# Performance work log

Hardware: AMD Instinct MI355X
Metric: run time of the kernel (lower is better)

Reference implementation:

```python
import jax, jax.numpy as jnp
import numpy as np

B, T, C = 8, 1024, 576
NH, NKV = 9, 3          # query heads, kv heads
HD = C // NH            # 64 head dim
KVC = C // NKV          # 192 kv proj width
N_REP = NH // NKV       # 3


def setup_inputs() -> dict:
    key = jax.random.key(0)
    ks = jax.random.split(key, 9)
    s = 0.02
    return {
        "x": jax.random.normal(ks[0], (B, T, C), jnp.float32),
        "Wq": jax.random.normal(ks[1], (C, C), jnp.float32) * s,
        "bq": jax.random.normal(ks[2], (C,), jnp.float32) * s,
        "Wk": jax.random.normal(ks[3], (C, KVC), jnp.float32) * s,
        "bk": jax.random.normal(ks[4], (KVC,), jnp.float32) * s,
        "Wv": jax.random.normal(ks[5], (C, KVC), jnp.float32) * s,
        "bv": jax.random.normal(ks[6], (KVC,), jnp.float32) * s,
        "Wo": jax.random.normal(ks[7], (C, C), jnp.float32) * s,
        "bo": jax.random.normal(ks[8], (C,), jnp.float32) * s,
    }


def reference(x, Wq, bq, Wk, bk, Wv, bv, Wo, bo):
    Bx, Tx, Cx = x.shape
    q = x @ Wq + bq                                # [B,T,C]
    k = x @ Wk + bk                                # [B,T,KVC]
    v = x @ Wv + bv
    # split heads: q -> [B,NH,T,HD]; k,v -> [B,NKV,T,HD]
    q = q.reshape(Bx, Tx, NH, HD).transpose(0, 2, 1, 3)
    k = k.reshape(Bx, Tx, NKV, HD).transpose(0, 2, 1, 3)
    v = v.reshape(Bx, Tx, NKV, HD).transpose(0, 2, 1, 3)
    # repeat_kv: [B,NKV,T,HD] -> [B,NKV*N_REP,T,HD]
    k = jnp.repeat(k, N_REP, axis=1)
    v = jnp.repeat(v, N_REP, axis=1)
    att = jnp.einsum("bhqd,bhkd->bhqk", q, k) * (1.0 / np.sqrt(HD))
    mask = jnp.tril(jnp.ones((Tx, Tx), bool))
    att = jnp.where(mask, att, -jnp.inf)
    att = jax.nn.softmax(att, axis=-1)
    y = jnp.einsum("bhqk,bhkd->bhqd", att, v)      # [B,NH,T,HD]
    y = y.transpose(0, 2, 1, 3).reshape(Bx, Tx, Cx)
    return y @ Wo + bo
```

## Files before the change

### kernel.cpp

```cpp
#include <hip/hip_runtime.h>
#include <hip/hip_bf16.h>
#include <math.h>

#define B_    8
#define T_    1024
#define C_    576
#define NH_   9
#define NKV_  3
#define HD_   64
#define KVC_  192
#define NREP_ 3
#define NQKV_ 960
#define NTK_  9

typedef __attribute__((ext_vector_type(8))) short bf16x8;
typedef __attribute__((ext_vector_type(4))) float f32x4;
typedef __attribute__((ext_vector_type(4))) int i32x4;

#define MFMA_16x16x32(a, b, c) __builtin_amdgcn_mfma_f32_16x16x32_bf16((a), (b), (c), 0, 0, 0)

__device__ __forceinline__ ushort f2bf(float f) {
  __hip_bfloat16 h = __float2bfloat16(f);
  return *reinterpret_cast<const ushort*>(&h);
}

__device__ __forceinline__ float fexp2(float x) { return __builtin_amdgcn_exp2f(x); }

__device__ __forceinline__ int swz(int row, int col) {
  int byte = (row << 7) + (col << 1);
  return (byte ^ ((row & 7) << 4)) >> 1;
}

__device__ __forceinline__ void gload16(const ushort* g, ushort* l) {
  __builtin_amdgcn_global_load_lds(
      (const __attribute__((address_space(1))) unsigned int*)g,
      (__attribute__((address_space(3))) unsigned int*)l, 16, 0, 0);
}

__device__ __forceinline__ i32x4 packrow(const float* src) {
  const float4 a = *reinterpret_cast<const float4*>(src);
  const float4 b = *reinterpret_cast<const float4*>(src + 4);
  union { ushort u[8]; i32x4 v; } t;
  t.u[0] = f2bf(a.x); t.u[1] = f2bf(a.y); t.u[2] = f2bf(a.z); t.u[3] = f2bf(a.w);
  t.u[4] = f2bf(b.x); t.u[5] = f2bf(b.y); t.u[6] = f2bf(b.z); t.u[7] = f2bf(b.w);
  return t.v;
}

__global__ __launch_bounds__(256) void convert_x_kernel(
    const float* __restrict__ x, ushort* __restrict__ xbt) {
  const int tm = blockIdx.x, tk = blockIdx.y;
  ushort* dst = xbt + ((size_t)tm * NTK_ + tk) * 8192;
  #pragma unroll
  for (int i = 0; i < 4; i++) {
    const int c = threadIdx.x + i * 256;
    const int row = c >> 3, colb = (c & 7) * 8;
    *reinterpret_cast<i32x4*>(&dst[swz(row, colb)]) =
        packrow(x + (size_t)(tm * 128 + row) * C_ + tk * 64 + colb);
  }
}

__global__ __launch_bounds__(256) void convert_w_kernel(
    const float* __restrict__ Wq, const float* __restrict__ Wk,
    const float* __restrict__ Wv, const float* __restrict__ Wo,
    const float* __restrict__ bq, const float* __restrict__ bk,
    const float* __restrict__ bv, const float* __restrict__ bo,
    ushort* __restrict__ wqkvT, ushort* __restrict__ woT, float* __restrict__ bcat) {
  const int tnc = blockIdx.x, tk = blockIdx.y;
  #pragma unroll
  for (int i = 0; i < 2; i++) {
    const int c = threadIdx.x + i * 256;
    const int row = c >> 3, colb = (c & 7) * 8;
    const float* src; int ld; ushort* dst; int ncol;
    if (tnc < 15) {
      const int n = tnc * 64 + row;
      if (n < 576)      { src = Wq; ld = C_;  ncol = n; }
      else if (n < 768) { src = Wk; ld = KVC_; ncol = n - 576; }
      else              { src = Wv; ld = KVC_; ncol = n - 768; }
      dst = wqkvT + ((size_t)tnc * NTK_ + tk) * 4096;
    } else {
      src = Wo; ld = C_; ncol = (tnc - 15) * 64 + row;
      dst = woT + ((size_t)(tnc - 15) * NTK_ + tk) * 4096;
    }
    union { ushort u[8]; i32x4 v; } t;
    #pragma unroll
    for (int e = 0; e < 8; e++)
      t.u[e] = f2bf(src[(size_t)(tk * 64 + colb + e) * ld + ncol]);
    *reinterpret_cast<i32x4*>(&dst[swz(row, colb)]) = t.v;
    if (tk == 0 && (c & 7) == 0) {
      const int n = tnc * 64 + row;
      float bv_;
      if (n < 576)       bv_ = bq[n];
      else if (n < 768)  bv_ = bk[n - 576];
      else if (n < 960)  bv_ = bv[n - 768];
      else               bv_ = bo[n - 960];
      bcat[n] = bv_;
    }
  }
}

template<int MODE>
__global__ __launch_bounds__(256) void gemm_lds_kernel(
    const ushort* __restrict__ At, const ushort* __restrict__ Bt,
    const float* __restrict__ bias, void* __restrict__ Cp,
    ushort* __restrict__ ktv, ushort* __restrict__ vtv, int N) {
  const int nwg = gridDim.x * gridDim.y;
  const int flat = blockIdx.y * gridDim.x + blockIdx.x;
  const int wg = (flat & 7) * (nwg >> 3) + (flat >> 3);
  const int bxs = wg % gridDim.x, bys = wg / gridDim.x;

  __shared__ ushort As[128 * 64];
  __shared__ ushort Bs[64 * 64];
  const int bm = bys * 128, bn = bxs * 64;
  const int tid = threadIdx.x;
  const int wave = tid >> 6, lane = tid & 63;
  const int lg = lane >> 4, ll = lane & 15;
  const int wm = (wave >> 1) * 64, wn = (wave & 1) * 32;
  f32x4 acc[4][2] = {};

  const ushort* abase = At + (size_t)bys * NTK_ * 8192;
  const ushort* bbase = Bt + (size_t)bxs * NTK_ * 4096;

  for (int kt = 0; kt < NTK_; kt++) {
    const ushort* ak = abase + (size_t)kt * 8192;
    const ushort* bk = bbase + (size_t)kt * 4096;
    #pragma unroll
    for (int i = 0; i < 4; i++) {
      const int c0 = (wave << 6) + (i << 8);
      gload16(ak + (size_t)(c0 + lane) * 8, &As[c0 * 8]);
    }
    #pragma unroll
    for (int i = 0; i < 2; i++) {
      const int c0 = (wave << 6) + (i << 8);
      gload16(bk + (size_t)(c0 + lane) * 8, &Bs[c0 * 8]);
    }
    __syncthreads();

    bf16x8 af[4][2], bfr[2][2];
    #pragma unroll
    for (int mt = 0; mt < 4; mt++) {
      af[mt][0] = *reinterpret_cast<const bf16x8*>(&As[swz(wm + mt * 16 + ll, lg * 8)]);
      af[mt][1] = *reinterpret_cast<const bf16x8*>(&As[swz(wm + mt * 16 + ll, 32 + lg * 8)]);
    }
    #pragma unroll
    for (int nt = 0; nt < 2; nt++) {
      bfr[nt][0] = *reinterpret_cast<const bf16x8*>(&Bs[swz(wn + nt * 16 + ll, lg * 8)]);
      bfr[nt][1] = *reinterpret_cast<const bf16x8*>(&Bs[swz(wn + nt * 16 + ll, 32 + lg * 8)]);
    }
    #pragma unroll
    for (int mt = 0; mt < 4; mt++) {
      #pragma unroll
      for (int nt = 0; nt < 2; nt++) {
        acc[mt][nt] = MFMA_16x16x32(af[mt][0], bfr[nt][0], acc[mt][nt]);
        acc[mt][nt] = MFMA_16x16x32(af[mt][1], bfr[nt][1], acc[mt][nt]);
      }
    }
    __syncthreads();
  }

  #pragma unroll
  for (int mt = 0; mt < 4; mt++) {
    #pragma unroll
    for (int nt = 0; nt < 2; nt++) {
      const int col = bn + wn + nt * 16 + ll;
      #pragma unroll
      for (int r = 0; r < 4; r++) {
        const int row = bm + wm + mt * 16 + lg * 4 + r;
        const float val = acc[mt][nt][r] + bias[col];
        if (MODE == 0) {
          ((float*)Cp)[(size_t)row * N + col] = val;
        } else {
          if (col < 576) {
            ((ushort*)Cp)[(size_t)row * C_ + col] = f2bf(val * 0.18033688011112042f);
          } else if (col < 768) {
            const int kvh = (col - 576) >> 6, d = (col - 576) & 63;
            ushort* t = ktv + (((size_t)(row >> 10) * 3 + kvh) * 16 + ((row >> 6) & 15)) * 4096;
            t[swz(row & 63, d)] = f2bf(val);
          } else {
            const int kvh = (col - 768) >> 6, d = (col - 768) & 63;
            ushort* t = vtv + (((size_t)(row >> 10) * 3 + kvh) * 16 + ((row >> 6) & 15)) * 4096;
            t[swz(d, row & 63)] = f2bf(val);
          }
        }
      }
    }
  }
}

__global__ __launch_bounds__(256) void attn_mfma_kernel(
    const ushort* __restrict__ qb, const ushort* __restrict__ ktv,
    const ushort* __restrict__ vtv, ushort* __restrict__ yt) {
  const int qt = 15 - blockIdx.z, h = blockIdx.x, b = blockIdx.y;
  const int kvh = h / NREP_;
  const int tid = threadIdx.x;
  const int wave = tid >> 6, lane = tid & 63;
  const int lg = lane >> 4, ll = lane & 15;
  const int w16 = wave << 4;
  const int qrow0 = qt << 6;
  const int ntile = qt + 1;

  __shared__ ushort Ks[2][4096];
  __shared__ ushort Vts[2][4096];
  __shared__ ushort Ps[4][1024];

  const ushort* ktb = ktv + ((size_t)b * 3 + kvh) * 16 * 4096;
  const ushort* vtb = vtv + ((size_t)b * 3 + kvh) * 16 * 4096;

  const ushort* qrow = qb + (size_t)(b * T_ + qrow0 + w16 + ll) * C_ + h * HD_;
  const bf16x8 qa0 = *reinterpret_cast<const bf16x8*>(qrow + lg * 8);
  const bf16x8 qa1 = *reinterpret_cast<const bf16x8*>(qrow + 32 + lg * 8);

  f32x4 o[4] = {};
  float m_i = -INFINITY, l_i = 0.f;

  {
    const ushort* ks = ktb;
    const ushort* vs = vtb;
    #pragma unroll
    for (int i = 0; i < 2; i++) {
      const int c0 = (wave << 6) + (i << 8);
      gload16(ks + (size_t)(c0 + lane) * 8, &Ks[0][c0 * 8]);
      gload16(vs + (size_t)(c0 + lane) * 8, &Vts[0][c0 * 8]);
    }
  }

  #pragma unroll 1
  for (int t = 0; t < ntile; t++) {
    const int cur = t & 1;
    if (t + 1 < ntile) {
      const ushort* ks = ktb + (size_t)(t + 1) * 4096;
      const ushort* vs = vtb + (size_t)(t + 1) * 4096;
      #pragma unroll
      for (int i = 0; i < 2; i++) {
        const int c0 = (wave << 6) + (i << 8);
        gload16(ks + (size_t)(c0 + lane) * 8, &Ks[cur ^ 1][c0 * 8]);
        gload16(vs + (size_t)(c0 + lane) * 8, &Vts[cur ^ 1][c0 * 8]);
      }
      asm volatile("s_waitcnt vmcnt(4)" ::: "memory");
    } else {
      asm volatile("s_waitcnt vmcnt(0)" ::: "memory");
    }
    __builtin_amdgcn_s_barrier();

    f32x4 s[4];
    #pragma unroll
    for (int kcl = 0; kcl < 4; kcl++) {
      const bf16x8 kb0 = *reinterpret_cast<const bf16x8*>(&Ks[cur][swz(kcl * 16 + ll, lg * 8)]);
      const bf16x8 kb1 = *reinterpret_cast<const bf16x8*>(&Ks[cur][swz(kcl * 16 + ll, 32 + lg * 8)]);
      f32x4 z = {};
      z = MFMA_16x16x32(kb0, qa0, z);
      s[kcl] = MFMA_16x16x32(kb1, qa1, z);
    }

    if (t == ntile - 1) {
      const int qg = qrow0 + w16 + ll - (t << 6);
      #pragma unroll
      for (int kcl = 0; kcl < 4; kcl++)
        #pragma unroll
        for (int r = 0; r < 4; r++)
          if (kcl * 16 + lg * 4 + r > qg) s[kcl][r] = -INFINITY;
    }

    float mA[4];
    #pragma unroll
    for (int kcl = 0; kcl < 4; kcl++)
      mA[kcl] = fmaxf(fmaxf(s[kcl][0], s[kcl][1]), fmaxf(s[kcl][2], s[kcl][3]));
    float t0 = fmaxf(fmaxf(mA[0], mA[1]), fmaxf(mA[2], mA[3]));
    t0 = fmaxf(t0, __shfl_xor(t0, 16));
    t0 = fmaxf(t0, __shfl_xor(t0, 32));
    if (!__all(t0 <= m_i + 11.5415603f)) {
      const float mn = fmaxf(m_i, t0);
      const float al = fexp2(m_i - mn);
      m_i = mn;
      l_i *= al;
      #pragma unroll
      for (int r = 0; r < 4; r++) {
        const float ar = __shfl(al, lg * 4 + r);
        o[0][r] *= ar; o[1][r] *= ar; o[2][r] *= ar; o[3][r] *= ar;
      }
    }

    float rk[4];
    ushort* Pw = Ps[wave];
    #pragma unroll
    for (int kcl = 0; kcl < 4; kcl++) {
      float p0 = fexp2(s[kcl][0] - m_i);
      float p1 = fexp2(s[kcl][1] - m_i);
      float p2 = fexp2(s[kcl][2] - m_i);
      float p3 = fexp2(s[kcl][3] - m_i);
      rk[kcl] = (p0 + p1) + (p2 + p3);
      uint w01 = (uint)f2bf(p0) | ((uint)f2bf(p1) << 16);
      uint w23 = (uint)f2bf(p2) | ((uint)f2bf(p3) << 16);
      *reinterpret_cast<uint*>(&Pw[swz(ll, kcl * 16 + lg * 4)])     = w01;
      *reinterpret_cast<uint*>(&Pw[swz(ll, kcl * 16 + lg * 4 + 2)]) = w23;
    }
    #pragma unroll
    for (int khl = 0; khl < 2; khl++) {
      const bf16x8 pa = *reinterpret_cast<const bf16x8*>(&Pw[swz(ll, khl * 32 + lg * 8)]);
      #pragma unroll
      for (int d0 = 0; d0 < 4; d0++) {
        const bf16x8 vbr = *reinterpret_cast<const bf16x8*>(&Vts[cur][swz(d0 * 16 + ll, khl * 32 + lg * 8)]);
        o[d0] = MFMA_16x16x32(pa, vbr, o[d0]);
      }
    }
    float rs = (rk[0] + rk[1]) + (rk[2] + rk[3]);
    rs += __shfl_xor(rs, 16);
    rs += __shfl_xor(rs, 32);
    l_i += rs;

    __builtin_amdgcn_s_barrier();
  }

  #pragma unroll
  for (int r = 0; r < 4; r++) {
    const float lr = __shfl(l_i, lg * 4 + r);
    const float inv = 1.f / lr;
    const int rowg = b * T_ + qrow0 + w16 + lg * 4 + r;
    ushort* ybase = yt + ((size_t)(rowg >> 7) * NTK_ + h) * 8192;
    const int lrow = rowg & 127;
    #pragma unroll
    for (int d0 = 0; d0 < 4; d0++) {
      ybase[swz(lrow, d0 * 16 + ll)] = f2bf(o[d0][r] * inv);
    }
  }
}

extern "C" void kernel_launch(void* const* d_in, const int* in_sizes, int n_in,
                              void* d_out, int out_size, void* d_ws, size_t ws_size,
                              hipStream_t stream) {
  const float* x  = (const float*)d_in[0];
  const float* Wq = (const float*)d_in[1];
  const float* bq = (const float*)d_in[2];
  const float* Wk = (const float*)d_in[3];
  const float* bk = (const float*)d_in[4];
  const float* Wv = (const float*)d_in[5];
  const float* bv = (const float*)d_in[6];
  const float* Wo = (const float*)d_in[7];
  const float* bo = (const float*)d_in[8];
  float* out = (float*)d_out;

  const int M = B_ * T_;
  ushort* wqkvT = (ushort*)d_ws;
  ushort* woT   = wqkvT + (size_t)15 * NTK_ * 4096;
  float*  bcat  = (float*)(woT + (size_t)9 * NTK_ * 4096);
  ushort* qb    = (ushort*)(bcat + 1536);
  ushort* ktv   = qb + (size_t)M * C_;
  ushort* vtv   = ktv + (size_t)B_ * NKV_ * 16 * 4096;
  ushort* yt    = vtv + (size_t)B_ * NKV_ * 16 * 4096;
  ushort* xbt   = yt + (size_t)M * C_;

  convert_w_kernel<<<dim3(24, NTK_), 256, 0, stream>>>(Wq, Wk, Wv, Wo, bq, bk, bv, bo,
                                                       wqkvT, woT, bcat);
  convert_x_kernel<<<dim3(M / 128, NTK_), 256, 0, stream>>>(x, xbt);
  gemm_lds_kernel<1><<<dim3(NQKV_ / 64, M / 128), 256, 0, stream>>>(
      xbt, wqkvT, bcat, qb, ktv, vtv, NQKV_);
  attn_mfma_kernel<<<dim3(NH_, B_, 16), 256, 0, stream>>>(qb, ktv, vtv, yt);
  gemm_lds_kernel<0><<<dim3(C_ / 64, M / 128), 256, 0, stream>>>(
      yt, woT, bcat + NQKV_, out, nullptr, nullptr, C_);
}
```

Before: 70.65 us.

## Double-buffer LDS tiles in projection GEMM to overlap loads with MFMA

```diff
diff --git a/kernel.cpp b/kernel.cpp
--- a/kernel.cpp
+++ b/kernel.cpp
@@ -108,8 +108,8 @@
   const int wg = (flat & 7) * (nwg >> 3) + (flat >> 3);
   const int bxs = wg % gridDim.x, bys = wg / gridDim.x;
 
-  __shared__ ushort As[128 * 64];
-  __shared__ ushort Bs[64 * 64];
+  __shared__ ushort As[2][128 * 64];
+  __shared__ ushort Bs[2][64 * 64];
   const int bm = bys * 128, bn = bxs * 64;
   const int tid = threadIdx.x;
   const int wave = tid >> 6, lane = tid & 63;
@@ -120,31 +120,50 @@
   const ushort* abase = At + (size_t)bys * NTK_ * 8192;
   const ushort* bbase = Bt + (size_t)bxs * NTK_ * 4096;
 
-  for (int kt = 0; kt < NTK_; kt++) {
-    const ushort* ak = abase + (size_t)kt * 8192;
-    const ushort* bk = bbase + (size_t)kt * 4096;
+  {
     #pragma unroll
     for (int i = 0; i < 4; i++) {
       const int c0 = (wave << 6) + (i << 8);
-      gload16(ak + (size_t)(c0 + lane) * 8, &As[c0 * 8]);
+      gload16(abase + (size_t)(c0 + lane) * 8, &As[0][c0 * 8]);
     }
     #pragma unroll
     for (int i = 0; i < 2; i++) {
       const int c0 = (wave << 6) + (i << 8);
-      gload16(bk + (size_t)(c0 + lane) * 8, &Bs[c0 * 8]);
-    }
-    __syncthreads();
+      gload16(bbase + (size_t)(c0 + lane) * 8, &Bs[0][c0 * 8]);
+    }
+  }
+
+  for (int kt = 0; kt < NTK_; kt++) {
+    const int cur = kt & 1;
+    if (kt + 1 < NTK_) {
+      const ushort* ak = abase + (size_t)(kt + 1) * 8192;
+      const ushort* bk = bbase + (size_t)(kt + 1) * 4096;
+      #pragma unroll
+      for (int i = 0; i < 4; i++) {
+        const int c0 = (wave << 6) + (i << 8);
+        gload16(ak + (size_t)(c0 + lane) * 8, &As[cur ^ 1][c0 * 8]);
+      }
+      #pragma unroll
+      for (int i = 0; i < 2; i++) {
+        const int c0 = (wave << 6) + (i << 8);
+        gload16(bk + (size_t)(c0 + lane) * 8, &Bs[cur ^ 1][c0 * 8]);
+      }
+      asm volatile("s_waitcnt vmcnt(6)" ::: "memory");
+    } else {
+      asm volatile("s_waitcnt vmcnt(0)" ::: "memory");
+    }
+    __builtin_amdgcn_s_barrier();
 
     bf16x8 af[4][2], bfr[2][2];
     #pragma unroll
     for (int mt = 0; mt < 4; mt++) {
-      af[mt][0] = *reinterpret_cast<const bf16x8*>(&As[swz(wm + mt * 16 + ll, lg * 8)]);
-      af[mt][1] = *reinterpret_cast<const bf16x8*>(&As[swz(wm + mt * 16 + ll, 32 + lg * 8)]);
+      af[mt][0] = *reinterpret_cast<const bf16x8*>(&As[cur][swz(wm + mt * 16 + ll, lg * 8)]);
+      af[mt][1] = *reinterpret_cast<const bf16x8*>(&As[cur][swz(wm + mt * 16 + ll, 32 + lg * 8)]);
     }
     #pragma unroll
     for (int nt = 0; nt < 2; nt++) {
-      bfr[nt][0] = *reinterpret_cast<const bf16x8*>(&Bs[swz(wn + nt * 16 + ll, lg * 8)]);
-      bfr[nt][1] = *reinterpret_cast<const bf16x8*>(&Bs[swz(wn + nt * 16 + ll, 32 + lg * 8)]);
+      bfr[nt][0] = *reinterpret_cast<const bf16x8*>(&Bs[cur][swz(wn + nt * 16 + ll, lg * 8)]);
+      bfr[nt][1] = *reinterpret_cast<const bf16x8*>(&Bs[cur][swz(wn + nt * 16 + ll, 32 + lg * 8)]);
     }
     #pragma unroll
     for (int mt = 0; mt < 4; mt++) {
@@ -154,7 +173,7 @@
         acc[mt][nt] = MFMA_16x16x32(af[mt][1], bfr[nt][1], acc[mt][nt]);
       }
     }
-    __syncthreads();
+    __builtin_amdgcn_s_barrier();
   }
 
   #pragma unroll
```

Result: no change. 71.13 us (+0.7%).

## Fuse conversion kernels and remap attention blocks for per-XCD KV locality

Applied to the files above, without the earlier changes.

```diff
diff --git a/kernel.cpp b/kernel.cpp
--- a/kernel.cpp
+++ b/kernel.cpp
@@ -46,54 +46,57 @@
   return t.v;
 }
 
-__global__ __launch_bounds__(256) void convert_x_kernel(
-    const float* __restrict__ x, ushort* __restrict__ xbt) {
-  const int tm = blockIdx.x, tk = blockIdx.y;
-  ushort* dst = xbt + ((size_t)tm * NTK_ + tk) * 8192;
-  #pragma unroll
-  for (int i = 0; i < 4; i++) {
-    const int c = threadIdx.x + i * 256;
-    const int row = c >> 3, colb = (c & 7) * 8;
-    *reinterpret_cast<i32x4*>(&dst[swz(row, colb)]) =
-        packrow(x + (size_t)(tm * 128 + row) * C_ + tk * 64 + colb);
-  }
-}
-
-__global__ __launch_bounds__(256) void convert_w_kernel(
+__global__ __launch_bounds__(256) void convert_all_kernel(
+    const float* __restrict__ x,
     const float* __restrict__ Wq, const float* __restrict__ Wk,
     const float* __restrict__ Wv, const float* __restrict__ Wo,
     const float* __restrict__ bq, const float* __restrict__ bk,
     const float* __restrict__ bv, const float* __restrict__ bo,
-    ushort* __restrict__ wqkvT, ushort* __restrict__ woT, float* __restrict__ bcat) {
-  const int tnc = blockIdx.x, tk = blockIdx.y;
-  #pragma unroll
-  for (int i = 0; i < 2; i++) {
-    const int c = threadIdx.x + i * 256;
-    const int row = c >> 3, colb = (c & 7) * 8;
-    const float* src; int ld; ushort* dst; int ncol;
-    if (tnc < 15) {
-      const int n = tnc * 64 + row;
-      if (n < 576)      { src = Wq; ld = C_;  ncol = n; }
-      else if (n < 768) { src = Wk; ld = KVC_; ncol = n - 576; }
-      else              { src = Wv; ld = KVC_; ncol = n - 768; }
-      dst = wqkvT + ((size_t)tnc * NTK_ + tk) * 4096;
-    } else {
-      src = Wo; ld = C_; ncol = (tnc - 15) * 64 + row;
-      dst = woT + ((size_t)(tnc - 15) * NTK_ + tk) * 4096;
-    }
-    union { ushort u[8]; i32x4 v; } t;
-    #pragma unroll
-    for (int e = 0; e < 8; e++)
-      t.u[e] = f2bf(src[(size_t)(tk * 64 + colb + e) * ld + ncol]);
-    *reinterpret_cast<i32x4*>(&dst[swz(row, colb)]) = t.v;
-    if (tk == 0 && (c & 7) == 0) {
-      const int n = tnc * 64 + row;
-      float bv_;
-      if (n < 576)       bv_ = bq[n];
-      else if (n < 768)  bv_ = bk[n - 576];
-      else if (n < 960)  bv_ = bv[n - 768];
-      else               bv_ = bo[n - 960];
-      bcat[n] = bv_;
+    ushort* __restrict__ wqkvT, ushort* __restrict__ woT, float* __restrict__ bcat,
+    ushort* __restrict__ xbt) {
+  const int bid = blockIdx.x;
+  if (bid < 216) {
+    const int tnc = bid / 9, tk = bid % 9;
+    #pragma unroll
+    for (int i = 0; i < 2; i++) {
+      const int c = threadIdx.x + i * 256;
+      const int row = c >> 3, colb = (c & 7) * 8;
+      const float* src; int ld; ushort* dst; int ncol;
+      if (tnc < 15) {
+        const int n = tnc * 64 + row;
+        if (n < 576)      { src = Wq; ld = C_;  ncol = n; }
+        else if (n < 768) { src = Wk; ld = KVC_; ncol = n - 576; }
+        else              { src = Wv; ld = KVC_; ncol = n - 768; }
+        dst = wqkvT + ((size_t)tnc * NTK_ + tk) * 4096;
+      } else {
+        src = Wo; ld = C_; ncol = (tnc - 15) * 64 + row;
+        dst = woT + ((size_t)(tnc - 15) * NTK_ + tk) * 4096;
+      }
+      union { ushort u[8]; i32x4 v; } t;
+      #pragma unroll
+      for (int e = 0; e < 8; e++)
+        t.u[e] = f2bf(src[(size_t)(tk * 64 + colb + e) * ld + ncol]);
+      *reinterpret_cast<i32x4*>(&dst[swz(row, colb)]) = t.v;
+      if (tk == 0 && (c & 7) == 0) {
+        const int n = tnc * 64 + row;
+        float bv_;
+        if (n < 576)       bv_ = bq[n];
+        else if (n < 768)  bv_ = bk[n - 576];
+        else if (n < 960)  bv_ = bv[n - 768];
+        else               bv_ = bo[n - 960];
+        bcat[n] = bv_;
+      }
+    }
+  } else {
+    const int r = bid - 216;
+    const int tm = r / 9, tk = r % 9;
+    ushort* dst = xbt + ((size_t)tm * NTK_ + tk) * 8192;
+    #pragma unroll
+    for (int i = 0; i < 4; i++) {
+      const int c = threadIdx.x + i * 256;
+      const int row = c >> 3, colb = (c & 7) * 8;
+      *reinterpret_cast<i32x4*>(&dst[swz(row, colb)]) =
+          packrow(x + (size_t)(tm * 128 + row) * C_ + tk * 64 + colb);
     }
   }
 }
@@ -189,8 +192,14 @@
 __global__ __launch_bounds__(256) void attn_mfma_kernel(
     const ushort* __restrict__ qb, const ushort* __restrict__ ktv,
     const ushort* __restrict__ vtv, ushort* __restrict__ yt) {
-  const int qt = 15 - blockIdx.z, h = blockIdx.x, b = blockIdx.y;
-  const int kvh = h / NREP_;
+  const int f = blockIdx.x + NH_ * (blockIdx.y + B_ * blockIdx.z);
+  const int xcd = f & 7, chunk = f >> 3;
+  const int g = xcd * 3 + chunk / 48;
+  const int within = chunk % 48;
+  const int b = g & 7, kvh = g >> 3;
+  const int h = kvh * 3 + within % 3;
+  const int qt = 15 - within / 3;
+
   const int tid = threadIdx.x;
   const int wave = tid >> 6, lane = tid & 63;
   const int lg = lane >> 4, ll = lane & 15;
@@ -213,13 +222,11 @@
   float m_i = -INFINITY, l_i = 0.f;
 
   {
-    const ushort* ks = ktb;
-    const ushort* vs = vtb;
     #pragma unroll
     for (int i = 0; i < 2; i++) {
       const int c0 = (wave << 6) + (i << 8);
-      gload16(ks + (size_t)(c0 + lane) * 8, &Ks[0][c0 * 8]);
-      gload16(vs + (size_t)(c0 + lane) * 8, &Vts[0][c0 * 8]);
+      gload16(ktb + (size_t)(c0 + lane) * 8, &Ks[0][c0 * 8]);
+      gload16(vtb + (size_t)(c0 + lane) * 8, &Vts[0][c0 * 8]);
     }
   }
 
@@ -348,9 +355,8 @@
   ushort* yt    = vtv + (size_t)B_ * NKV_ * 16 * 4096;
   ushort* xbt   = yt + (size_t)M * C_;
 
-  convert_w_kernel<<<dim3(24, NTK_), 256, 0, stream>>>(Wq, Wk, Wv, Wo, bq, bk, bv, bo,
-                                                       wqkvT, woT, bcat);
-  convert_x_kernel<<<dim3(M / 128, NTK_), 256, 0, stream>>>(x, xbt);
+  convert_all_kernel<<<dim3(216 + 576), 256, 0, stream>>>(
+      x, Wq, Wk, Wv, Wo, bq, bk, bv, bo, wqkvT, woT, bcat, xbt);
   gemm_lds_kernel<1><<<dim3(NQKV_ / 64, M / 128), 256, 0, stream>>>(
       xbt, wqkvT, bcat, qb, ktv, vtv, NQKV_);
   attn_mfma_kernel<<<dim3(NH_, B_, 16), 256, 0, stream>>>(qb, ktv, vtv, yt);
```

Measured after the change: 73.86 us. 1.05x slower.

## Make attention kernel persistent with an atomic work queue, heaviest tiles first

Applied to the files above, without the earlier changes.

```diff
diff --git a/kernel.cpp b/kernel.cpp
--- a/kernel.cpp
+++ b/kernel.cpp
@@ -12,6 +12,7 @@
 #define NREP_ 3
 #define NQKV_ 960
 #define NTK_  9
+#define NITEM_ 1152
 
 typedef __attribute__((ext_vector_type(8))) short bf16x8;
 typedef __attribute__((ext_vector_type(4))) float f32x4;
@@ -64,8 +65,10 @@
     const float* __restrict__ Wv, const float* __restrict__ Wo,
     const float* __restrict__ bq, const float* __restrict__ bk,
     const float* __restrict__ bv, const float* __restrict__ bo,
-    ushort* __restrict__ wqkvT, ushort* __restrict__ woT, float* __restrict__ bcat) {
+    ushort* __restrict__ wqkvT, ushort* __restrict__ woT, float* __restrict__ bcat,
+    uint* __restrict__ qcount) {
   const int tnc = blockIdx.x, tk = blockIdx.y;
+  if (tnc == 0 && tk == 0 && threadIdx.x == 0) *qcount = 0u;
   #pragma unroll
   for (int i = 0; i < 2; i++) {
     const int c = threadIdx.x + i * 256;
@@ -188,138 +191,145 @@
 
 __global__ __launch_bounds__(256) void attn_mfma_kernel(
     const ushort* __restrict__ qb, const ushort* __restrict__ ktv,
-    const ushort* __restrict__ vtv, ushort* __restrict__ yt) {
-  const int qt = 15 - blockIdx.z, h = blockIdx.x, b = blockIdx.y;
-  const int kvh = h / NREP_;
+    const ushort* __restrict__ vtv, ushort* __restrict__ yt,
+    uint* __restrict__ qcount) {
   const int tid = threadIdx.x;
   const int wave = tid >> 6, lane = tid & 63;
   const int lg = lane >> 4, ll = lane & 15;
   const int w16 = wave << 4;
-  const int qrow0 = qt << 6;
-  const int ntile = qt + 1;
 
   __shared__ ushort Ks[2][4096];
   __shared__ ushort Vts[2][4096];
   __shared__ ushort Ps[4][1024];
-
-  const ushort* ktb = ktv + ((size_t)b * 3 + kvh) * 16 * 4096;
-  const ushort* vtb = vtv + ((size_t)b * 3 + kvh) * 16 * 4096;
-
-  const ushort* qrow = qb + (size_t)(b * T_ + qrow0 + w16 + ll) * C_ + h * HD_;
-  const bf16x8 qa0 = *reinterpret_cast<const bf16x8*>(qrow + lg * 8);
-  const bf16x8 qa1 = *reinterpret_cast<const bf16x8*>(qrow + 32 + lg * 8);
-
-  f32x4 o[4] = {};
-  float m_i = -INFINITY, l_i = 0.f;
-
-  {
-    const ushort* ks = ktb;
-    const ushort* vs = vtb;
+  __shared__ uint witem;
+
+  while (true) {
+    if (tid == 0) witem = atomicAdd(qcount, 1u);
+    __syncthreads();
+    const uint w = witem;
+    if (w >= NITEM_) break;
+    const int qt = 15 - (int)(w / 72);
+    const int rem = (int)(w % 72);
+    const int h = rem % 9, b = rem / 9;
+    const int kvh = h / NREP_;
+    const int qrow0 = qt << 6;
+    const int ntile = qt + 1;
+
+    const ushort* ktb = ktv + ((size_t)b * 3 + kvh) * 16 * 4096;
+    const ushort* vtb = vtv + ((size_t)b * 3 + kvh) * 16 * 4096;
+
+    const ushort* qrow = qb + (size_t)(b * T_ + qrow0 + w16 + ll) * C_ + h * HD_;
+    const bf16x8 qa0 = *reinterpret_cast<const bf16x8*>(qrow + lg * 8);
+    const bf16x8 qa1 = *reinterpret_cast<const bf16x8*>(qrow + 32 + lg * 8);
+
+    f32x4 o[4] = {};
+    float m_i = -INFINITY, l_i = 0.f;
+
     #pragma unroll
     for (int i = 0; i < 2; i++) {
       const int c0 = (wave << 6) + (i << 8);
-      gload16(ks + (size_t)(c0 + lane) * 8, &Ks[0][c0 * 8]);
-      gload16(vs + (size_t)(c0 + lane) * 8, &Vts[0][c0 * 8]);
-    }
-  }
-
-  #pragma unroll 1
-  for (int t = 0; t < ntile; t++) {
-    const int cur = t & 1;
-    if (t + 1 < ntile) {
-      const ushort* ks = ktb + (size_t)(t + 1) * 4096;
-      const ushort* vs = vtb + (size_t)(t + 1) * 4096;
-      #pragma unroll
-      for (int i = 0; i < 2; i++) {
-        const int c0 = (wave << 6) + (i << 8);
-        gload16(ks + (size_t)(c0 + lane) * 8, &Ks[cur ^ 1][c0 * 8]);
-        gload16(vs + (size_t)(c0 + lane) * 8, &Vts[cur ^ 1][c0 * 8]);
-      }
-      asm volatile("s_waitcnt vmcnt(4)" ::: "memory");
-    } else {
-      asm volatile("s_waitcnt vmcnt(0)" ::: "memory");
-    }
-    __builtin_amdgcn_s_barrier();
-
-    f32x4 s[4];
-    #pragma unroll
-    for (int kcl = 0; kcl < 4; kcl++) {
-      const bf16x8 kb0 = *reinterpret_cast<const bf16x8*>(&Ks[cur][swz(kcl * 16 + ll, lg * 8)]);
-      const bf16x8 kb1 = *reinterpret_cast<const bf16x8*>(&Ks[cur][swz(kcl * 16 + ll, 32 + lg * 8)]);
-      f32x4 z = {};
-      z = MFMA_16x16x32(kb0, qa0, z);
-      s[kcl] = MFMA_16x16x32(kb1, qa1, z);
-    }
-
-    if (t == ntile - 1) {
-      const int qg = qrow0 + w16 + ll - (t << 6);
+      gload16(ktb + (size_t)(c0 + lane) * 8, &Ks[0][c0 * 8]);
+      gload16(vtb + (size_t)(c0 + lane) * 8, &Vts[0][c0 * 8]);
+    }
+
+    #pragma unroll 1
+    for (int t = 0; t < ntile; t++) {
+      const int cur = t & 1;
+      if (t + 1 < ntile) {
+        const ushort* ks = ktb + (size_t)(t + 1) * 4096;
+        const ushort* vs = vtb + (size_t)(t + 1) * 4096;
+        #pragma unroll
+        for (int i = 0; i < 2; i++) {
+          const int c0 = (wave << 6) + (i << 8);
+          gload16(ks + (size_t)(c0 + lane) * 8, &Ks[cur ^ 1][c0 * 8]);
+          gload16(vs + (size_t)(c0 + lane) * 8, &Vts[cur ^ 1][c0 * 8]);
+        }
+        asm volatile("s_waitcnt vmcnt(4)" ::: "memory");
+      } else {
+        asm volatile("s_waitcnt vmcnt(0)" ::: "memory");
+      }
+      __builtin_amdgcn_s_barrier();
+
+      f32x4 s[4];
+      #pragma unroll
+      for (int kcl = 0; kcl < 4; kcl++) {
+        const bf16x8 kb0 = *reinterpret_cast<const bf16x8*>(&Ks[cur][swz(kcl * 16 + ll, lg * 8)]);
+        const bf16x8 kb1 = *reinterpret_cast<const bf16x8*>(&Ks[cur][swz(kcl * 16 + ll, 32 + lg * 8)]);
+        f32x4 z = {};
+        z = MFMA_16x16x32(kb0, qa0, z);
+        s[kcl] = MFMA_16x16x32(kb1, qa1, z);
+      }
+
+      if (t == ntile - 1) {
+        const int qg = qrow0 + w16 + ll - (t << 6);
+        #pragma unroll
+        for (int kcl = 0; kcl < 4; kcl++)
+          #pragma unroll
+          for (int r = 0; r < 4; r++)
+            if (kcl * 16 + lg * 4 + r > qg) s[kcl][r] = -INFINITY;
+      }
+
+      float mA[4];
       #pragma unroll
       for (int kcl = 0; kcl < 4; kcl++)
+        mA[kcl] = fmaxf(fmaxf(s[kcl][0], s[kcl][1]), fmaxf(s[kcl][2], s[kcl][3]));
+      float t0 = fmaxf(fmaxf(mA[0], mA[1]), fmaxf(mA[2], mA[3]));
+      t0 = fmaxf(t0, __shfl_xor(t0, 16));
+      t0 = fmaxf(t0, __shfl_xor(t0, 32));
+      if (!__all(t0 <= m_i + 11.5415603f)) {
+        const float mn = fmaxf(m_i, t0);
+        const float al = fexp2(m_i - mn);
+        m_i = mn;
+        l_i *= al;
         #pragma unroll
-        for (int r = 0; r < 4; r++)
-          if (kcl * 16 + lg * 4 + r > qg) s[kcl][r] = -INFINITY;
-    }
-
-    float mA[4];
-    #pragma unroll
-    for (int kcl = 0; kcl < 4; kcl++)
-      mA[kcl] = fmaxf(fmaxf(s[kcl][0], s[kcl][1]), fmaxf(s[kcl][2], s[kcl][3]));
-    float t0 = fmaxf(fmaxf(mA[0], mA[1]), fmaxf(mA[2], mA[3]));
-    t0 = fmaxf(t0, __shfl_xor(t0, 16));
-    t0 = fmaxf(t0, __shfl_xor(t0, 32));
-    if (!__all(t0 <= m_i + 11.5415603f)) {
-      const float mn = fmaxf(m_i, t0);
-      const float al = fexp2(m_i - mn);
-      m_i = mn;
-      l_i *= al;
-      #pragma unroll
-      for (int r = 0; r < 4; r++) {
-        const float ar = __shfl(al, lg * 4 + r);
-        o[0][r] *= ar; o[1][r] *= ar; o[2][r] *= ar; o[3][r] *= ar;
-      }
-    }
-
-    float rk[4];
-    ushort* Pw = Ps[wave];
-    #pragma unroll
-    for (int kcl = 0; kcl < 4; kcl++) {
-      float p0 = fexp2(s[kcl][0] - m_i);
-      float p1 = fexp2(s[kcl][1] - m_i);
-      float p2 = fexp2(s[kcl][2] - m_i);
-      float p3 = fexp2(s[kcl][3] - m_i);
-      rk[kcl] = (p0 + p1) + (p2 + p3);
-      uint w01 = (uint)f2bf(p0) | ((uint)f2bf(p1) << 16);
-      uint w23 = (uint)f2bf(p2) | ((uint)f2bf(p3) << 16);
-      *reinterpret_cast<uint*>(&Pw[swz(ll, kcl * 16 + lg * 4)])     = w01;
-      *reinterpret_cast<uint*>(&Pw[swz(ll, kcl * 16 + lg * 4 + 2)]) = w23;
-    }
-    #pragma unroll
-    for (int khl = 0; khl < 2; khl++) {
-      const bf16x8 pa = *reinterpret_cast<const bf16x8*>(&Pw[swz(ll, khl * 32 + lg * 8)]);
+        for (int r = 0; r < 4; r++) {
+          const float ar = __shfl(al, lg * 4 + r);
+          o[0][r] *= ar; o[1][r] *= ar; o[2][r] *= ar; o[3][r] *= ar;
+        }
+      }
+
+      float rk[4];
+      ushort* Pw = Ps[wave];
+      #pragma unroll
+      for (int kcl = 0; kcl < 4; kcl++) {
+        float p0 = fexp2(s[kcl][0] - m_i);
+        float p1 = fexp2(s[kcl][1] - m_i);
+        float p2 = fexp2(s[kcl][2] - m_i);
+        float p3 = fexp2(s[kcl][3] - m_i);
+        rk[kcl] = (p0 + p1) + (p2 + p3);
+        uint w01 = (uint)f2bf(p0) | ((uint)f2bf(p1) << 16);
+        uint w23 = (uint)f2bf(p2) | ((uint)f2bf(p3) << 16);
+        *reinterpret_cast<uint*>(&Pw[swz(ll, kcl * 16 + lg * 4)])     = w01;
+        *reinterpret_cast<uint*>(&Pw[swz(ll, kcl * 16 + lg * 4 + 2)]) = w23;
+      }
+      #pragma unroll
+      for (int khl = 0; khl < 2; khl++) {
+        const bf16x8 pa = *reinterpret_cast<const bf16x8*>(&Pw[swz(ll, khl * 32 + lg * 8)]);
+        #pragma unroll
+        for (int d0 = 0; d0 < 4; d0++) {
+          const bf16x8 vbr = *reinterpret_cast<const bf16x8*>(&Vts[cur][swz(d0 * 16 + ll, khl * 32 + lg * 8)]);
+          o[d0] = MFMA_16x16x32(pa, vbr, o[d0]);
+        }
+      }
+      float rs = (rk[0] + rk[1]) + (rk[2] + rk[3]);
+      rs += __shfl_xor(rs, 16);
+      rs += __shfl_xor(rs, 32);
+      l_i += rs;
+
+      __builtin_amdgcn_s_barrier();
+    }
+
+    #pragma unroll
+    for (int r = 0; r < 4; r++) {
+      const float lr = __shfl(l_i, lg * 4 + r);
+      const float inv = 1.f / lr;
+      const int rowg = b * T_ + qrow0 + w16 + lg * 4 + r;
+      ushort* ybase = yt + ((size_t)(rowg >> 7) * NTK_ + h) * 8192;
+      const int lrow = rowg & 127;
       #pragma unroll
       for (int d0 = 0; d0 < 4; d0++) {
-        const bf16x8 vbr = *reinterpret_cast<const bf16x8*>(&Vts[cur][swz(d0 * 16 + ll, khl * 32 + lg * 8)]);
-        o[d0] = MFMA_16x16x32(pa, vbr, o[d0]);
-      }
-    }
-    float rs = (rk[0] + rk[1]) + (rk[2] + rk[3]);
-    rs += __shfl_xor(rs, 16);
-    rs += __shfl_xor(rs, 32);
-    l_i += rs;
-
-    __builtin_amdgcn_s_barrier();
-  }
-
-  #pragma unroll
-  for (int r = 0; r < 4; r++) {
-    const float lr = __shfl(l_i, lg * 4 + r);
-    const float inv = 1.f / lr;
-    const int rowg = b * T_ + qrow0 + w16 + lg * 4 + r;
-    ushort* ybase = yt + ((size_t)(rowg >> 7) * NTK_ + h) * 8192;
-    const int lrow = rowg & 127;
-    #pragma unroll
-    for (int d0 = 0; d0 < 4; d0++) {
-      ybase[swz(lrow, d0 * 16 + ll)] = f2bf(o[d0][r] * inv);
+        ybase[swz(lrow, d0 * 16 + ll)] = f2bf(o[d0][r] * inv);
+      }
     }
   }
 }
@@ -347,13 +357,14 @@
   ushort* vtv   = ktv + (size_t)B_ * NKV_ * 16 * 4096;
   ushort* yt    = vtv + (size_t)B_ * NKV_ * 16 * 4096;
   ushort* xbt   = yt + (size_t)M * C_;
+  uint*   qcnt  = (uint*)(xbt + (size_t)M * C_);
 
   convert_w_kernel<<<dim3(24, NTK_), 256, 0, stream>>>(Wq, Wk, Wv, Wo, bq, bk, bv, bo,
-                                                       wqkvT, woT, bcat);
+                                                       wqkvT, woT, bcat, qcnt);
   convert_x_kernel<<<dim3(M / 128, NTK_), 256, 0, stream>>>(x, xbt);
   gemm_lds_kernel<1><<<dim3(NQKV_ / 64, M / 128), 256, 0, stream>>>(
       xbt, wqkvT, bcat, qb, ktv, vtv, NQKV_);
-  attn_mfma_kernel<<<dim3(NH_, B_, 16), 256, 0, stream>>>(qb, ktv, vtv, yt);
+  attn_mfma_kernel<<<dim3(1024), 256, 0, stream>>>(qb, ktv, vtv, yt, qcnt);
   gemm_lds_kernel<0><<<dim3(C_ / 64, M / 128), 256, 0, stream>>>(
       yt, woT, bcat + NQKV_, out, nullptr, nullptr, C_);
 }
```

Result: slower. 88.01 us (+24.6%).
